# Kernel optimization log

Measured on AMD Instinct MI355X. Metric: run time of the kernel, lower is better.

Reference implementation:

```python
import jax, jax.numpy as jnp
import numpy as np

NEG_BIG = -9e15
ALPHA = 0.2  # leaky relu slope


def setup_inputs() -> dict:
    key = jax.random.key(0)
    k_h, k_adj, k_W, k_a = jax.random.split(key, 4)
    N, F_in, F_out = 8192, 512, 64
    h = jax.random.normal(k_h, (N, F_in), dtype=jnp.float32)
    adj = jax.random.randint(k_adj, (N, N), 0, 2, dtype=jnp.int32)
    adj = adj.at[jnp.arange(N), jnp.arange(N)].set(1)  # self-loops (add_self_loops)
    # xavier_uniform with gain=1.414
    limW = 1.414 * np.sqrt(6.0 / (F_in + F_out))
    W = jax.random.uniform(k_W, (F_in, F_out), jnp.float32, -limW, limW)
    lima = 1.414 * np.sqrt(6.0 / (2 * F_out + 1))
    a = jax.random.uniform(k_a, (2 * F_out, 1), jnp.float32, -lima, lima)
    return {"h": h, "adj": adj, "W": W, "a": a}


def reference(h, adj, W, a):
    F_out = W.shape[1]
    Wh = h @ W                                  # [N, F_out]
    # a_input[i,j] = concat(Wh[i], Wh[j]); a_input @ a == Wh@a1 + (Wh@a2)^T
    a1, a2 = a[:F_out, 0], a[F_out:, 0]
    src = Wh @ a1                               # [N]
    dst = Wh @ a2                               # [N]
    e = jax.nn.leaky_relu(src[:, None] + dst[None, :], ALPHA)  # [N, N]
    att = jnp.where(adj > 0, e, NEG_BIG)
    att = jax.nn.softmax(att, axis=1)
    # dropout is identity in eval mode (training=False)
    return att @ Wh                             # [N, F_out]
```

## Files before the change

kernel.cpp:

```cpp
#include <hip/hip_runtime.h>
#include <hip/hip_bf16.h>

#define N 8192
#define FIN 512
#define FOUT 64
#define NW 256
#define L2E 1.44269504089f
#define SPLIT 16

typedef __attribute__((address_space(1))) const void* gas_cptr;
typedef __attribute__((address_space(3))) void* las_ptr;
typedef float f32x4 __attribute__((ext_vector_type(4)));
typedef short bf16x8 __attribute__((ext_vector_type(8)));

#if __has_builtin(__builtin_amdgcn_exp2f)
#define EXP2(x) __builtin_amdgcn_exp2f(x)
#else
#define EXP2(x) exp2f(x)
#endif

static __device__ __forceinline__ unsigned short f2bf_rne(float f) {
  unsigned u = __float_as_uint(f);
  u += 0x7FFFu + ((u >> 16) & 1u);
  return (unsigned short)(u >> 16);
}
static __device__ __forceinline__ unsigned fkey(float f) {
  unsigned u = __float_as_uint(f);
  return (u & 0x80000000u) ? ~u : (u | 0x80000000u);
}

__global__ __launch_bounds__(256) void k_pack(
    const int* __restrict__ adj, unsigned* __restrict__ mask) {
  const int t = threadIdx.x;
  const int w = t >> 6, ll = t & 63;
  const int row = blockIdx.x * 2 + (w >> 1);
  const int jbase = (w & 1) * (N / 2);
  const int* arow = adj + (size_t)row * N + jbase;
  unsigned* mrow = mask + (size_t)row * NW + (jbase >> 5);
#pragma unroll 1
  for (int it = 0; it < 64; it += 4) {
    int x0 = arow[(it + 0) * 64 + ll];
    int x1 = arow[(it + 1) * 64 + ll];
    int x2 = arow[(it + 2) * 64 + ll];
    int x3 = arow[(it + 3) * 64 + ll];
    unsigned long long b0 = __ballot(x0 != 0);
    unsigned long long b1 = __ballot(x1 != 0);
    unsigned long long b2 = __ballot(x2 != 0);
    unsigned long long b3 = __ballot(x3 != 0);
    if (ll == 0) {
      *reinterpret_cast<uint4*>(&mrow[it * 2]) =
          make_uint4((unsigned)b0, (unsigned)(b0 >> 32),
                     (unsigned)b1, (unsigned)(b1 >> 32));
      *reinterpret_cast<uint4*>(&mrow[it * 2 + 4]) =
          make_uint4((unsigned)b2, (unsigned)(b2 >> 32),
                     (unsigned)b3, (unsigned)(b3 >> 32));
    }
  }
}

__global__ __launch_bounds__(256) void k_wh(
    const float* __restrict__ h, const float* __restrict__ W,
    const float* __restrict__ a, unsigned short* __restrict__ WhT,
    float* __restrict__ src2, float* __restrict__ dst2,
    unsigned* __restrict__ dmaxk) {
  __shared__ __attribute__((aligned(16))) char wts[64 * 512 * 2];
  __shared__ __attribute__((aligned(16))) char hsb[2][64 * 64 * 2];

  const int t = threadIdx.x;
  const int w = t >> 6;
  const int ll = t & 63;
  const int lc = ll & 15;
  const int row0 = blockIdx.x * 64;

  {
    const int k0 = t * 2;
#pragma unroll
    for (int f4 = 0; f4 < 16; ++f4) {
      float4 x0 = *reinterpret_cast<const float4*>(&W[(size_t)k0 * FOUT + f4 * 4]);
      float4 x1 = *reinterpret_cast<const float4*>(&W[(size_t)(k0 + 1) * FOUT + f4 * 4]);
      const float e0[4] = {x0.x, x0.y, x0.z, x0.w};
      const float e1[4] = {x1.x, x1.y, x1.z, x1.w};
#pragma unroll
      for (int e = 0; e < 4; ++e) {
        int f = f4 * 4 + e;
        int bb = f * 1024 + k0 * 2;
        bb ^= (f & 7) << 4;
        *reinterpret_cast<ushort2*>(wts + bb) =
            make_ushort2(f2bf_rne(e0[e]), f2bf_rne(e1[e]));
      }
    }
  }
  __syncthreads();

  f32x4 acc[4];
#pragma unroll
  for (int c = 0; c < 4; ++c) acc[c] = (f32x4){0.f, 0.f, 0.f, 0.f};

  const int hrow = 16 * w + (ll >> 2);
  const float* hbase = &h[(size_t)(row0 + hrow) * FIN + (ll & 3) * 16];

#define LOADH(dst, kc)                                                        \
  do {                                                                        \
    dst[0] = *reinterpret_cast<const float4*>(hbase + (kc));                  \
    dst[1] = *reinterpret_cast<const float4*>(hbase + (kc) + 4);              \
    dst[2] = *reinterpret_cast<const float4*>(hbase + (kc) + 8);              \
    dst[3] = *reinterpret_cast<const float4*>(hbase + (kc) + 12);             \
  } while (0)

#define WRITEH(buf, src)                                                      \
  do {                                                                        \
    int bb0 = hrow * 128 + (ll & 3) * 32;                                     \
    bb0 ^= (hrow & 7) << 4;                                                   \
    _Pragma("unroll") for (int q = 0; q < 4; ++q) {                           \
      ushort4 u = make_ushort4(f2bf_rne(src[q].x), f2bf_rne(src[q].y),        \
                               f2bf_rne(src[q].z), f2bf_rne(src[q].w));       \
      *reinterpret_cast<ushort4*>(hsb[buf] + (bb0 ^ (q * 8))) = u;            \
    }                                                                         \
  } while (0)

#define MFMA_CHUNK(buf, kcb)                                                  \
  do {                                                                        \
    _Pragma("unroll") for (int k0 = 0; k0 < 2; ++k0) {                        \
      int arow = 16 * w + lc;                                                 \
      int ab = arow * 128 + k0 * 64 + ((ll >> 4) << 4);                       \
      ab ^= (arow & 7) << 4;                                                  \
      bf16x8 af = *reinterpret_cast<const bf16x8*>(hsb[buf] + ab);            \
      _Pragma("unroll") for (int c = 0; c < 4; ++c) {                         \
        int f = c * 16 + lc;                                                  \
        int bb = f * 1024 + (kcb) + k0 * 64 + ((ll >> 4) << 4);               \
        bb ^= (f & 7) << 4;                                                   \
        bf16x8 bfr = *reinterpret_cast<const bf16x8*>(wts + bb);              \
        acc[c] = __builtin_amdgcn_mfma_f32_16x16x32_bf16(af, bfr, acc[c], 0, 0, 0); \
      }                                                                       \
    }                                                                         \
  } while (0)

  float4 ha[4], hb[4];
  LOADH(ha, 0);
#pragma unroll
  for (int c2 = 0; c2 < 4; ++c2) {
    WRITEH(0, ha);
    LOADH(hb, (2 * c2 + 1) * 64);
    MFMA_CHUNK(0, (2 * c2) * 128);
    WRITEH(1, hb);
    if (c2 < 3) LOADH(ha, (2 * c2 + 2) * 64);
    MFMA_CHUNK(1, (2 * c2 + 1) * 128);
  }

  float a1v[4], a2v[4];
#pragma unroll
  for (int c = 0; c < 4; ++c) {
    a1v[c] = a[c * 16 + lc];
    a2v[c] = a[FOUT + c * 16 + lc];
  }
  float p1[4], p2[4];
#pragma unroll
  for (int q = 0; q < 4; ++q) {
    p1[q] = acc[0][q] * a1v[0] + acc[1][q] * a1v[1] + acc[2][q] * a1v[2] + acc[3][q] * a1v[3];
    p2[q] = acc[0][q] * a2v[0] + acc[1][q] * a2v[1] + acc[2][q] * a2v[2] + acc[3][q] * a2v[3];
  }
#pragma unroll
  for (int msk = 8; msk >= 1; msk >>= 1)
#pragma unroll
    for (int q = 0; q < 4; ++q) {
      p1[q] += __shfl_xor(p1[q], msk);
      p2[q] += __shfl_xor(p2[q], msk);
    }
#pragma unroll
  for (int q = 0; q < 4; ++q) { p1[q] *= L2E; p2[q] *= L2E; }

  const int r0 = row0 + 16 * w + ((ll >> 4) << 2);
  if (lc == 0) {
#pragma unroll
    for (int q = 0; q < 4; ++q) { src2[r0 + q] = p1[q]; dst2[r0 + q] = p2[q]; }
  }
#pragma unroll
  for (int c = 0; c < 4; ++c) {
    ushort4 u = make_ushort4(f2bf_rne(acc[c][0]), f2bf_rne(acc[c][1]),
                             f2bf_rne(acc[c][2]), f2bf_rne(acc[c][3]));
    *reinterpret_cast<ushort4*>(&WhT[(size_t)(c * 16 + lc) * N + r0]) = u;
  }
  float wm = fmaxf(fmaxf(p2[0], p2[1]), fmaxf(p2[2], p2[3]));
  wm = fmaxf(wm, __shfl_xor(wm, 16));
  wm = fmaxf(wm, __shfl_xor(wm, 32));
  if (ll == 0) atomicMax(dmaxk, fkey(wm));
#undef LOADH
#undef WRITEH
#undef MFMA_CHUNK
}

__global__ __launch_bounds__(256) void k_attn(
    const unsigned* __restrict__ mask, const unsigned short* __restrict__ WhT,
    const float* __restrict__ src2, const float* __restrict__ dst2,
    const unsigned* __restrict__ dmaxk, float* __restrict__ out,
    float* __restrict__ Opart, float* __restrict__ lpart, const int split) {
  __shared__ __attribute__((aligned(16))) char whs[2 * 8192];
  __shared__ __attribute__((aligned(16))) char pbs[8192];

  const int t = threadIdx.x;
  const int w = t >> 6;
  const int ll = t & 63;
  const int rg = t >> 4;
  const int cg = t & 15;
  const int i0 = rg * 4;
  const int row0 = blockIdx.x * 64;
  const int jlen = N / split;
  const int jbase = blockIdx.y * jlen;
  const int ntiles = jlen / 64;

  unsigned kk = dmaxk[0];
  const float dmax2 = (kk & 0x80000000u) ? __uint_as_float(kk & 0x7FFFFFFFu)
                                         : __uint_as_float(~kk);

  float s2v[4], m2[4], l[4];
#pragma unroll
  for (int r = 0; r < 4; ++r) {
    s2v[r] = src2[row0 + i0 + r];
    float x = s2v[r] + dmax2;
    m2[r] = fmaxf(x, 0.2f * x);
    l[r] = 0.f;
  }

  f32x4 acc[4];
#pragma unroll
  for (int c = 0; c < 4; ++c) acc[c] = (f32x4){0.f, 0.f, 0.f, 0.f};

#define STAGE_WHS(buf, j0)                                                    \
  do {                                                                        \
    _Pragma("unroll") for (int i_ = 0; i_ < 2; ++i_) {                        \
      int slot = t + i_ * 256;                                                \
      int b = slot * 16;                                                      \
      int u = b ^ (((b >> 7) & 7) << 4);                                      \
      int f_ = u >> 7;                                                        \
      int jl = (u & 127) >> 1;                                                \
      __builtin_amdgcn_global_load_lds(                                       \
          (gas_cptr)(WhT + (size_t)f_ * N + (j0) + jl),                       \
          (las_ptr)(whs + (buf)*8192 + b), 16, 0, 0);                         \
    }                                                                         \
  } while (0)

#define LOAD_MSK(MW, DV, j0)                                                  \
  do {                                                                        \
    int wi_ = ((j0) >> 5) + (cg >> 3);                                        \
    _Pragma("unroll") for (int r_ = 0; r_ < 4; ++r_)                          \
      MW[r_] = mask[(size_t)(row0 + i0 + r_) * NW + wi_];                     \
    float4 d_ = *reinterpret_cast<const float4*>(&dst2[(j0) + cg * 4]);       \
    DV[0] = d_.x; DV[1] = d_.y; DV[2] = d_.z; DV[3] = d_.w;                   \
  } while (0)

  unsigned mw[4], nmw[4];
  float dv[4], ndv[4];
  STAGE_WHS(0, jbase);
  LOAD_MSK(mw, dv, jbase);

  const int bsh = (cg & 7) * 4;

  for (int jt = 0; jt < ntiles; ++jt) {
    const int cur = jt & 1;
    __syncthreads();

    if (jt + 1 < ntiles) {
      STAGE_WHS(cur ^ 1, jbase + (jt + 1) * 64);
      LOAD_MSK(nmw, ndv, jbase + (jt + 1) * 64);
    }

    float p[4][4];
#pragma unroll
    for (int r = 0; r < 4; ++r) {
      unsigned b = mw[r] >> bsh;
#pragma unroll
      for (int jj = 0; jj < 4; ++jj) {
        float x = s2v[r] + dv[jj];
        float e2 = fmaxf(x, 0.2f * x);
        float pe = EXP2(e2 - m2[r]);
        pe = (b & (1u << jj)) ? pe : 0.f;
        p[r][jj] = pe;
        l[r] += pe;
      }
    }
#pragma unroll
    for (int r = 0; r < 4; ++r) {
      unsigned u0 = __float_as_uint(p[r][0]);
      unsigned u1 = __float_as_uint(p[r][1]);
      unsigned u2 = __float_as_uint(p[r][2]);
      unsigned u3 = __float_as_uint(p[r][3]);
      uint2 pk = make_uint2((u0 >> 16) | (u1 & 0xFFFF0000u),
                            (u2 >> 16) | (u3 & 0xFFFF0000u));
      int row = i0 + r;
      int ba = (row << 7) + (cg << 3);
      ba ^= (row & 7) << 4;
      *reinterpret_cast<uint2*>(pbs + ba) = pk;
    }

    {
      const int lc = ll & 15;
      const int g16 = (ll >> 4) << 4;
#pragma unroll
      for (int k0 = 0; k0 < 2; ++k0) {
        int arow = 16 * w + lc;
        int ab = (arow << 7) + k0 * 64 + g16;
        ab ^= (arow & 7) << 4;
        bf16x8 af = *reinterpret_cast<const bf16x8*>(pbs + ab);
#pragma unroll
        for (int c = 0; c < 4; ++c) {
          int brow = c * 16 + lc;
          int bb = (brow << 7) + k0 * 64 + g16;
          bb ^= (brow & 7) << 4;
          bf16x8 bfr = *reinterpret_cast<const bf16x8*>(whs + cur * 8192 + bb);
          acc[c] = __builtin_amdgcn_mfma_f32_16x16x32_bf16(af, bfr, acc[c], 0, 0, 0);
        }
      }
    }

    if (jt + 1 < ntiles) {
#pragma unroll
      for (int r = 0; r < 4; ++r) { mw[r] = nmw[r]; dv[r] = ndv[r]; }
    }
  }

#pragma unroll
  for (int msk = 8; msk >= 1; msk >>= 1)
#pragma unroll
    for (int r = 0; r < 4; ++r) l[r] += __shfl_xor(l[r], msk);

  const int orow = row0 + 16 * w + ((ll >> 4) << 2);
  const int ocol = ll & 15;
  if (split == 1) {
#pragma unroll
    for (int c = 0; c < 4; ++c)
#pragma unroll
      for (int q = 0; q < 4; ++q)
        out[(size_t)(orow + q) * FOUT + c * 16 + ocol] = acc[c][q] / l[q];
  } else {
    const int pb = blockIdx.y;
#pragma unroll
    for (int c = 0; c < 4; ++c)
#pragma unroll
      for (int q = 0; q < 4; ++q)
        Opart[((size_t)pb * N + orow + q) * FOUT + c * 16 + ocol] = acc[c][q];
    if (cg == 0) {
#pragma unroll
      for (int r = 0; r < 4; ++r)
        lpart[(size_t)pb * N + row0 + i0 + r] = l[r];
    }
  }
#undef STAGE_WHS
#undef LOAD_MSK
}

__global__ __launch_bounds__(256) void k_combine(
    const float* __restrict__ Opart, const float* __restrict__ lpart,
    float* __restrict__ out, const int split) {
  int idx = blockIdx.x * 256 + threadIdx.x;
  int row = idx >> 6;
  float num = 0.f, den = 0.f;
  for (int k = 0; k < split; ++k) {
    num += Opart[(size_t)k * N * FOUT + idx];
    den += lpart[(size_t)k * N + row];
  }
  out[idx] = num / den;
}

extern "C" void kernel_launch(void* const* d_in, const int* in_sizes, int n_in,
                              void* d_out, int out_size, void* d_ws, size_t ws_size,
                              hipStream_t stream) {
  const float* h = (const float*)d_in[0];
  const int* adj = (const int*)d_in[1];
  const float* W = (const float*)d_in[2];
  const float* a = (const float*)d_in[3];
  float* out = (float*)d_out;

  unsigned short* WhT = (unsigned short*)d_ws;
  float* src2 = (float*)(WhT + (size_t)FOUT * N);
  float* dst2 = src2 + N;
  unsigned* dmaxk = (unsigned*)(dst2 + N);
  unsigned* mask = dmaxk + 64;
  float* Opart = (float*)(mask + (size_t)N * NW);

  const size_t base_bytes = (size_t)FOUT * N * 2 + 2 * N * 4 + 256 +
                            (size_t)N * NW * 4;
  int split = SPLIT;
  while (split > 1 &&
         base_bytes + (size_t)split * ((size_t)N * FOUT + N) * 4 > ws_size)
    split >>= 1;
  float* lpart = Opart + (size_t)split * N * FOUT;

  hipMemsetAsync(dmaxk, 0, 4, stream);
  k_pack<<<dim3(N / 2), 256, 0, stream>>>(adj, mask);
  k_wh<<<dim3(N / 64), 256, 0, stream>>>(h, W, a, WhT, src2, dst2, dmaxk);
  k_attn<<<dim3(N / 64, split), 256, 0, stream>>>(mask, WhT, src2, dst2, dmaxk,
                                                  out, Opart, lpart, split);
  if (split > 1)
    k_combine<<<dim3((N * FOUT) / 256), 256, 0, stream>>>(Opart, lpart, out, split);
}
```

Measured before the change: 119.2 us.

## Load WhT MFMA fragments directly from global, dropping LDS staging and barriers

The attention kernel no longer stages WhT tiles into a double-buffered LDS area with global_load_lds. Each wave now reads its own bf16x8 B fragments for the MFMAs straight from global memory into registers. The per-tile __syncthreads goes away, since each wave writes and reads only its own rows of the probability buffer. This frees LDS and removes block-wide synchronisation, but all four waves now fetch the same WhT tile redundantly through the cache. Those loads are also issued in the same iteration that uses them, with no prefetch, so their latency may be exposed.

```diff
diff --git a/kernel.cpp b/kernel.cpp
--- a/kernel.cpp
+++ b/kernel.cpp
@@ -194,7 +194,6 @@
     const float* __restrict__ src2, const float* __restrict__ dst2,
     const unsigned* __restrict__ dmaxk, float* __restrict__ out,
     float* __restrict__ Opart, float* __restrict__ lpart, const int split) {
-  __shared__ __attribute__((aligned(16))) char whs[2 * 8192];
   __shared__ __attribute__((aligned(16))) char pbs[8192];
 
   const int t = threadIdx.x;
@@ -203,6 +202,9 @@
   const int rg = t >> 4;
   const int cg = t & 15;
   const int i0 = rg * 4;
+  const int lc = ll & 15;
+  const int g16 = (ll >> 4) << 4;
+  const int g8 = (ll >> 4) << 3;
   const int row0 = blockIdx.x * 64;
   const int jlen = N / split;
   const int jbase = blockIdx.y * jlen;
@@ -225,43 +227,37 @@
 #pragma unroll
   for (int c = 0; c < 4; ++c) acc[c] = (f32x4){0.f, 0.f, 0.f, 0.f};
 
-#define STAGE_WHS(buf, j0)                                                    \
-  do {                                                                        \
-    _Pragma("unroll") for (int i_ = 0; i_ < 2; ++i_) {                        \
-      int slot = t + i_ * 256;                                                \
-      int b = slot * 16;                                                      \
-      int u = b ^ (((b >> 7) & 7) << 4);                                      \
-      int f_ = u >> 7;                                                        \
-      int jl = (u & 127) >> 1;                                                \
-      __builtin_amdgcn_global_load_lds(                                       \
-          (gas_cptr)(WhT + (size_t)f_ * N + (j0) + jl),                       \
-          (las_ptr)(whs + (buf)*8192 + b), 16, 0, 0);                         \
-    }                                                                         \
-  } while (0)
-
-#define LOAD_MSK(MW, DV, j0)                                                  \
-  do {                                                                        \
-    int wi_ = ((j0) >> 5) + (cg >> 3);                                        \
-    _Pragma("unroll") for (int r_ = 0; r_ < 4; ++r_)                          \
-      MW[r_] = mask[(size_t)(row0 + i0 + r_) * NW + wi_];                     \
-    float4 d_ = *reinterpret_cast<const float4*>(&dst2[(j0) + cg * 4]);       \
-    DV[0] = d_.x; DV[1] = d_.y; DV[2] = d_.z; DV[3] = d_.w;                   \
-  } while (0)
+  const int bsh = (cg & 7) * 4;
+  const int wi0 = (jbase >> 5) + (cg >> 3);
 
   unsigned mw[4], nmw[4];
   float dv[4], ndv[4];
-  STAGE_WHS(0, jbase);
-  LOAD_MSK(mw, dv, jbase);
-
-  const int bsh = (cg & 7) * 4;
-
-  for (int jt = 0; jt < ntiles; ++jt) {
-    const int cur = jt & 1;
-    __syncthreads();
-
-    if (jt + 1 < ntiles) {
-      STAGE_WHS(cur ^ 1, jbase + (jt + 1) * 64);
-      LOAD_MSK(nmw, ndv, jbase + (jt + 1) * 64);
+#pragma unroll
+  for (int r = 0; r < 4; ++r)
+    mw[r] = mask[(size_t)(row0 + i0 + r) * NW + wi0];
+  {
+    float4 d_ = *reinterpret_cast<const float4*>(&dst2[jbase + cg * 4]);
+    dv[0] = d_.x; dv[1] = d_.y; dv[2] = d_.z; dv[3] = d_.w;
+  }
+
+#pragma unroll 1
+  for (int jt2 = 0; jt2 < ntiles; ++jt2) {
+    const int j0 = jbase + jt2 * 64;
+
+    bf16x8 bfr[2][4];
+#pragma unroll
+    for (int k0 = 0; k0 < 2; ++k0)
+#pragma unroll
+      for (int c = 0; c < 4; ++c)
+        bfr[k0][c] = *reinterpret_cast<const bf16x8*>(
+            &WhT[(size_t)(c * 16 + lc) * N + j0 + k0 * 32 + g8]);
+
+    if (jt2 + 1 < ntiles) {
+#pragma unroll
+      for (int r = 0; r < 4; ++r)
+        nmw[r] = mask[(size_t)(row0 + i0 + r) * NW + wi0 + 2 * (jt2 + 1)];
+      float4 d_ = *reinterpret_cast<const float4*>(&dst2[j0 + 64 + cg * 4]);
+      ndv[0] = d_.x; ndv[1] = d_.y; ndv[2] = d_.z; ndv[3] = d_.w;
     }
 
     float p[4][4];
@@ -292,27 +288,19 @@
       *reinterpret_cast<uint2*>(pbs + ba) = pk;
     }
 
-    {
-      const int lc = ll & 15;
-      const int g16 = (ll >> 4) << 4;
-#pragma unroll
-      for (int k0 = 0; k0 < 2; ++k0) {
-        int arow = 16 * w + lc;
-        int ab = (arow << 7) + k0 * 64 + g16;
-        ab ^= (arow & 7) << 4;
-        bf16x8 af = *reinterpret_cast<const bf16x8*>(pbs + ab);
-#pragma unroll
-        for (int c = 0; c < 4; ++c) {
-          int brow = c * 16 + lc;
-          int bb = (brow << 7) + k0 * 64 + g16;
-          bb ^= (brow & 7) << 4;
-          bf16x8 bfr = *reinterpret_cast<const bf16x8*>(whs + cur * 8192 + bb);
-          acc[c] = __builtin_amdgcn_mfma_f32_16x16x32_bf16(af, bfr, acc[c], 0, 0, 0);
-        }
-      }
-    }
-
-    if (jt + 1 < ntiles) {
+#pragma unroll
+    for (int k0 = 0; k0 < 2; ++k0) {
+      int arow = 16 * w + lc;
+      int ab = (arow << 7) + k0 * 64 + g16;
+      ab ^= (arow & 7) << 4;
+      bf16x8 af = *reinterpret_cast<const bf16x8*>(pbs + ab);
+#pragma unroll
+      for (int c = 0; c < 4; ++c)
+        acc[c] = __builtin_amdgcn_mfma_f32_16x16x32_bf16(af, bfr[k0][c],
+                                                         acc[c], 0, 0, 0);
+    }
+
+    if (jt2 + 1 < ntiles) {
 #pragma unroll
       for (int r = 0; r < 4; ++r) { mw[r] = nmw[r]; dv[r] = ndv[r]; }
     }
@@ -344,8 +332,6 @@
         lpart[(size_t)pb * N + row0 + i0 + r] = l[r];
     }
   }
-#undef STAGE_WHS
-#undef LOAD_MSK
 }
 
 __global__ __launch_bounds__(256) void k_combine(
```

Result: slower. 151.8 us (+27.3%).
